# Kernel optimization log

Measured on AMD Instinct MI355X. Metric: run time of the kernel, lower is better.

The kernel has to match this reference:

```python
import jax, jax.numpy as jnp
import numpy as np

NB_ATOMS = 1024
NB_CHANNELS = 3
ATOM_SIZE = 16
NONDIFF_STEPS = 30
DIFF_STEPS = 10
TEMP = 100.0
EPS = 1e-8
BATCH = 16384


def setup_inputs() -> dict:
    key = jax.random.key(0)
    k1, k2 = jax.random.split(key)
    y = jax.random.normal(k1, (BATCH, NB_CHANNELS, ATOM_SIZE, ATOM_SIZE), dtype=jnp.float32)
    # init='random': randn / (atom_size * sqrt(nb_channels))
    atoms = jax.random.normal(k2, (NB_ATOMS, NB_CHANNELS, ATOM_SIZE, ATOM_SIZE), dtype=jnp.float32)
    atoms = atoms / (ATOM_SIZE * np.sqrt(NB_CHANNELS).astype(np.float32))
    return {"y": y, "atoms": atoms}


def reference(y, atoms):
    B = y.shape[0]
    A = atoms.shape[0]
    # L1 norms per sample / per atom
    y_norms = jnp.sum(jnp.abs(y.reshape(B, -1)), axis=1).reshape(-1, 1, 1, 1)  # [B,1,1,1]
    a_flat = atoms.reshape(A, -1)
    a_flat = a_flat / jnp.sum(jnp.abs(a_flat), axis=1, keepdims=True)          # [A,D]

    X = a_flat @ a_flat.T                                   # [A,A] gram matrix
    q = a_flat @ (y / y_norms).reshape(B, -1).T             # [A,B]
    coeffs = jnp.full((A, B), 1.0 / A, dtype=y.dtype)

    Xs = jax.lax.stop_gradient(X)
    qs = jax.lax.stop_gradient(q)

    def nondiff_step(i, c):
        grad = Xs @ c - qs                                  # [A,B]
        # faithful to torch: argmin over the BATCH dim, scatter one 1 per atom row
        am = jnp.zeros_like(c).at[jnp.arange(A), jnp.argmin(grad, axis=1)].set(1.0)
        d = am - c
        denom = jnp.sum(d * (Xs @ d)) + EPS                 # scalar (as in torch)
        lam = jnp.clip(-jnp.sum(d * grad, axis=0)[None, :] / denom, 0.0, 1.0)
        return c + d * lam

    coeffs = jax.lax.fori_loop(0, NONDIFF_STEPS, nondiff_step, coeffs)
    coeffs = jax.lax.stop_gradient(coeffs)

    def diff_step(c, _):
        grad = X @ c - q
        sm = jax.nn.softmax(-TEMP * grad, axis=0)           # softmax over atoms
        d = sm - c
        denom = jnp.sum(d * (X @ d)) + EPS
        lam = jnp.clip(-jnp.sum(d * grad, axis=0)[None, :] / denom, 0.0, 1.0)
        return c + d * lam, None

    coeffs, _ = jax.lax.scan(diff_step, coeffs, None, length=DIFF_STEPS)

    # einsum 'ij,ilmn->jlmn' with normalized atoms, rescale by y L1 norms
    recon = (coeffs.T @ a_flat).reshape(B, NB_CHANNELS, ATOM_SIZE, ATOM_SIZE) * y_norms
    return recon
```

## Files before the change

kernel.cpp:

```cpp
#include <hip/hip_runtime.h>
#include <hip/hip_bf16.h>
#include <math.h>

#define A_DIM 1024
#define D_DIM 768
#define B_DIM 16384
#define TEMP_C 100.0f
#define EPS_C 1e-8f


typedef __attribute__((ext_vector_type(8))) short short8;
typedef __attribute__((ext_vector_type(4))) float f32x4;
#define MFMA16(a, b, c) __builtin_amdgcn_mfma_f32_16x16x32_bf16(a, b, c, 0, 0, 0)

typedef __attribute__((address_space(3))) unsigned char lds_byte;
typedef __attribute__((address_space(1))) const unsigned char g_byte;
__device__ __forceinline__ void async_copy16(const void* gptr, void* lptr) {
    __builtin_amdgcn_global_load_lds((g_byte*)gptr, (lds_byte*)lptr, 16, 0, 0);
}

#define SCHED0 __builtin_amdgcn_sched_barrier(0)
#define ASM_BAR asm volatile("s_barrier" ::: "memory")

__device__ __forceinline__ void swz(int i, int& m0, int& n0) {
    int xcd = i & 7, j = i >> 3;
    m0 = ((xcd << 4) + (j >> 3)) << 7;
    n0 = (j & 7) << 7;
}


__device__ __forceinline__ float wave_sum(float v) {
#pragma unroll
    for (int m = 1; m < 64; m <<= 1) v += __shfl_xor(v, m);
    return v;
}
__device__ __forceinline__ float wave_max(float v) {
#pragma unroll
    for (int m = 1; m < 64; m <<= 1) v = fmaxf(v, __shfl_xor(v, m));
    return v;
}

__device__ __forceinline__ float block_reduce_sum(float v, float* red) {
    int t = threadIdx.x;
    v = wave_sum(v);
    if ((t & 63) == 0) red[t >> 6] = v;
    __syncthreads();
    float r = red[0] + red[1] + red[2] + red[3];
    __syncthreads();
    return r;
}

__device__ __forceinline__ float block_reduce_max(float v, float* red) {
    int t = threadIdx.x;
    v = wave_max(v);
    if ((t & 63) == 0) red[t >> 6] = v;
    __syncthreads();
    float r = fmaxf(fmaxf(red[0], red[1]), fmaxf(red[2], red[3]));
    __syncthreads();
    return r;
}

__device__ __forceinline__ void block_reduce_sum3(float& a, float& b, float& c, float* red) {
    int t = threadIdx.x;
    a = wave_sum(a);
    b = wave_sum(b);
    c = wave_sum(c);
    if ((t & 63) == 0) {
        int w = t >> 6;
        red[w] = a; red[4 + w] = b; red[8 + w] = c;
    }
    __syncthreads();
    a = red[0] + red[1] + red[2] + red[3];
    b = red[4] + red[5] + red[6] + red[7];
    c = red[8] + red[9] + red[10] + red[11];
    __syncthreads();
}


__device__ __forceinline__ unsigned int fkey(float v) {
    unsigned int u = __float_as_uint(v);
    return u ^ ((u & 0x80000000u) ? 0xFFFFFFFFu : 0x80000000u);
}

__device__ __forceinline__ unsigned short f2bf(float x) {
    unsigned int u = __float_as_uint(x);
    return (unsigned short)((u + 0x7FFFu + ((u >> 16) & 1u)) >> 16);
}
__device__ __forceinline__ float bf2f(unsigned short h) {
    return __uint_as_float(((unsigned int)h) << 16);
}
__device__ __forceinline__ void split2(float x, unsigned short& hi, unsigned short& lo) {
    hi = f2bf(x);
    lo = f2bf(x - bf2f(hi));
}


__device__ __forceinline__ void stage_tile8(const unsigned short* gsrc, int stride, int k0,
                                            unsigned short* ltile, int lane) {
    int srow = lane >> 2;
    int scol = (lane & 3) * 8;
#pragma unroll
    for (int s = 0; s < 8; s++) {
        const unsigned short* src = gsrc + (size_t)(s * 16 + srow) * stride + k0 + scol;
        async_copy16(src, ltile + s * 512);
    }
}

__device__ __forceinline__ void mfma_k32(const unsigned short* lds, int wm, int wn, int lane,
                                         f32x4 acc[4][4]) {
    int frow = lane & 15, fk = (lane >> 4) * 8;
    short8 ah[4], al[4], bh[4], bl[4];
#pragma unroll
    for (int t = 0; t < 4; t++) {
        int ar = (wm * 64 + t * 16 + frow) * 32 + fk;
        ah[t] = *(const short8*)&lds[ar];
        al[t] = *(const short8*)&lds[4096 + ar];
        int br = (wn * 64 + t * 16 + frow) * 32 + fk;
        bh[t] = *(const short8*)&lds[8192 + br];
        bl[t] = *(const short8*)&lds[12288 + br];
    }
#pragma unroll
    for (int i = 0; i < 4; i++)
#pragma unroll
        for (int j = 0; j < 4; j++) {
            acc[i][j] = MFMA16(ah[i], bh[j], acc[i][j]);
            acc[i][j] = MFMA16(ah[i], bl[j], acc[i][j]);
            acc[i][j] = MFMA16(al[i], bh[j], acc[i][j]);
        }
}


template <int PART>
__device__ __forceinline__ void stage_part(unsigned short* buf,
                                           const unsigned short* Ahi,
                                           const unsigned short* Alo,
                                           const unsigned short* Xhi,
                                           const unsigned short* Xlo,
                                           int m0, int n0, int k0, int t) {
    constexpr int AHI = 0;
    constexpr int ALO = 8192;
    constexpr int BHI = 16384;
    constexpr int BLO = 24576;
    int r = t >> 2;
    int cg = (t & 3) ^ ((t >> 3) & 3);
    size_t col = (size_t)k0 + cg * 8;
    if constexpr (PART == 0) {
        async_copy16(Ahi + (size_t)(m0 + r) * A_DIM + col,       buf + AHI + t * 8);
        async_copy16(Ahi + (size_t)(m0 + 128 + r) * A_DIM + col, buf + AHI + 4096 + t * 8);
    } else if constexpr (PART == 1) {
        async_copy16(Alo + (size_t)(m0 + r) * A_DIM + col,       buf + ALO + t * 8);
        async_copy16(Alo + (size_t)(m0 + 128 + r) * A_DIM + col, buf + ALO + 4096 + t * 8);
    } else if constexpr (PART == 2) {
        async_copy16(Xhi + (size_t)(n0 + r) * A_DIM + col,       buf + BHI + t * 8);
        async_copy16(Xhi + (size_t)(n0 + 128 + r) * A_DIM + col, buf + BHI + 4096 + t * 8);
    } else {
        async_copy16(Xlo + (size_t)(n0 + r) * A_DIM + col,       buf + BLO + t * 8);
        async_copy16(Xlo + (size_t)(n0 + 128 + r) * A_DIM + col, buf + BLO + 4096 + t * 8);
    }
}

__device__ __forceinline__ void mfma_mi3(short8 ah, short8 al,
                                         const short8 bh[4], const short8 bl[4],
                                         f32x4* accRow) {
#pragma unroll
    for (int j = 0; j < 4; j++) {
        accRow[j] = MFMA16(ah, bh[j], accRow[j]);
        accRow[j] = MFMA16(ah, bl[j], accRow[j]);
        accRow[j] = MFMA16(al, bh[j], accRow[j]);
    }
}

template <int MODE>
__global__ __launch_bounds__(512, 2) void gemm256(const unsigned short* __restrict__ Ahi,
                                                  const unsigned short* __restrict__ Alo,
                                                  const unsigned short* __restrict__ Xhi,
                                                  const unsigned short* __restrict__ Xlo,
                                                  const float* __restrict__ qt,
                                                  unsigned long long* __restrict__ keys,
                                                  float* __restrict__ cxc,
                                                  float* __restrict__ cq,
                                                  float* __restrict__ scal,
                                                  float* __restrict__ G,
                                                  float* __restrict__ scal3,
                                                  float* __restrict__ XC) {
    constexpr int BUFS = 32768;
    constexpr int AHI = 0;
    constexpr int ALO = 8192;
    constexpr int BHI = 16384;
    constexpr int BLO = 24576;
    __shared__ unsigned short lds[2 * BUFS];
    __shared__ float red[8];
    int tid = threadIdx.x;
    if (MODE == 0 && blockIdx.x == 0 && tid < 4) scal[tid] = 0.f;
    int w = tid >> 6, lane = tid & 63;
    int wm = w >> 2, wn = w & 3;
    int bi = blockIdx.x;
    int xcd = bi & 7, bj = bi >> 3;
    int m0 = ((xcd << 3) + (bj >> 2)) << 8;
    int n0 = (bj & 3) << 8;

    f32x4 acc[8][4];
#pragma unroll
    for (int i = 0; i < 8; i++)
#pragma unroll
        for (int j = 0; j < 4; j++) acc[i][j] = f32x4{0.f, 0.f, 0.f, 0.f};

    int frow = lane & 15;
    int sw = ((lane >> 4) ^ ((frow >> 1) & 3)) * 8;

    stage_part<0>(lds, Ahi, Alo, Xhi, Xlo, m0, n0, 0, tid);
    stage_part<1>(lds, Ahi, Alo, Xhi, Xlo, m0, n0, 0, tid);
    stage_part<2>(lds, Ahi, Alo, Xhi, Xlo, m0, n0, 0, tid);
    stage_part<3>(lds, Ahi, Alo, Xhi, Xlo, m0, n0, 0, tid);

    int cur = 0;
    for (int ks = 0; ks < 32; ++ks) {
        unsigned short* rb = lds + cur * BUFS;
        unsigned short* wb = lds + (cur ^ 1) * BUFS;
        const bool pf = (ks < 31);
        const int k1 = (ks + 1) * 32;

        if (pf) {
            stage_part<0>(wb, Ahi, Alo, Xhi, Xlo, m0, n0, k1, tid);
            SCHED0;
            asm volatile("s_waitcnt vmcnt(2)" ::: "memory");
        } else {
            asm volatile("s_waitcnt vmcnt(0)" ::: "memory");
        }
        SCHED0; ASM_BAR; SCHED0;

        short8 bh[4], bl[4];
#pragma unroll
        for (int j = 0; j < 4; j++) {
            int br = wn * 64 + j * 16 + frow;
            bh[j] = *(const short8*)&rb[BHI + br * 32 + sw];
            bl[j] = *(const short8*)&rb[BLO + br * 32 + sw];
        }
        {
            int ar0 = wm * 128 + 0 * 16 + frow, ar1 = wm * 128 + 1 * 16 + frow;
            short8 a0h = *(const short8*)&rb[AHI + ar0 * 32 + sw];
            short8 a1h = *(const short8*)&rb[AHI + ar1 * 32 + sw];
            short8 a0l = *(const short8*)&rb[ALO + ar0 * 32 + sw];
            short8 a1l = *(const short8*)&rb[ALO + ar1 * 32 + sw];
            if (pf) stage_part<1>(wb, Ahi, Alo, Xhi, Xlo, m0, n0, k1, tid);
            SCHED0; ASM_BAR; SCHED0;
            asm volatile("s_waitcnt lgkmcnt(0)" ::: "memory"); SCHED0;
            __builtin_amdgcn_s_setprio(1);
            mfma_mi3(a0h, a0l, bh, bl, acc[0]);
            mfma_mi3(a1h, a1l, bh, bl, acc[1]);
            __builtin_amdgcn_s_setprio(0);
            SCHED0; ASM_BAR; SCHED0;
        }
#pragma unroll
        for (int ph = 1; ph < 4; ph++) {
            int mia = 2 * ph, mib = 2 * ph + 1;
            int ara = wm * 128 + mia * 16 + frow, arb = wm * 128 + mib * 16 + frow;
            short8 aah = *(const short8*)&rb[AHI + ara * 32 + sw];
            short8 abh = *(const short8*)&rb[AHI + arb * 32 + sw];
            short8 aal = *(const short8*)&rb[ALO + ara * 32 + sw];
            short8 abl = *(const short8*)&rb[ALO + arb * 32 + sw];
            if (pf) {
                if (ph == 1) stage_part<2>(wb, Ahi, Alo, Xhi, Xlo, m0, n0, k1, tid);
                if (ph == 2) stage_part<3>(wb, Ahi, Alo, Xhi, Xlo, m0, n0, k1, tid);
            }
            SCHED0; ASM_BAR; SCHED0;
            asm volatile("s_waitcnt lgkmcnt(0)" ::: "memory"); SCHED0;
            __builtin_amdgcn_s_setprio(1);
            mfma_mi3(aah, aal, bh, bl, acc[mia]);
            mfma_mi3(abh, abl, bh, bl, acc[mib]);
            __builtin_amdgcn_s_setprio(0);
            SCHED0; ASM_BAR; SCHED0;
        }
        cur ^= 1;
    }

    int crow = (lane >> 4) * 4, ccol = lane & 15;
    if constexpr (MODE == 0) {
        unsigned long long best[4] = {~0ULL, ~0ULL, ~0ULL, ~0ULL};
#pragma unroll
        for (int mi = 0; mi < 8; mi++)
#pragma unroll
            for (int r = 0; r < 4; r++) {
                int gm = m0 + wm * 128 + mi * 16 + crow + r;
                float pcx = 0.f, pcq = 0.f;
#pragma unroll
                for (int jj = 0; jj < 4; jj++) {
                    int gn = n0 + wn * 64 + jj * 16 + ccol;
                    size_t idx = (size_t)gm * A_DIM + gn;
                    float c = bf2f(Ahi[idx]) + bf2f(Alo[idx]);
                    float q = qt[idx];
                    float xc = acc[mi][jj][r];
                    XC[idx] = xc;
                    pcx += c * xc;
                    pcq += c * q;
                    unsigned long long key =
                        ((unsigned long long)fkey(xc - q) << 32) | (unsigned int)gm;
                    if (key < best[jj]) best[jj] = key;
                }
                for (int mm = 1; mm < 16; mm <<= 1) {
                    pcx += __shfl_xor(pcx, mm, 16);
                    pcq += __shfl_xor(pcq, mm, 16);
                }
                if (ccol == 0) {
                    atomicAdd(&cxc[gm], pcx);
                    atomicAdd(&cq[gm], pcq);
                }
            }
#pragma unroll
        for (int jj = 0; jj < 4; jj++) {
            int gn = n0 + wn * 64 + jj * 16 + ccol;
            unsigned long long o = __shfl_xor(best[jj], 16);
            if (o < best[jj]) best[jj] = o;
            o = __shfl_xor(best[jj], 32);
            if (o < best[jj]) best[jj] = o;
            if ((lane >> 4) == 0) atomicMin(&keys[gn], best[jj]);
        }
    } else {
        float part = 0.f;
#pragma unroll
        for (int mi = 0; mi < 8; mi++)
#pragma unroll
            for (int r = 0; r < 4; r++) {
                int gm = m0 + wm * 128 + mi * 16 + crow + r;
#pragma unroll
                for (int jj = 0; jj < 4; jj++) {
                    int gn = n0 + wn * 64 + jj * 16 + ccol;
                    size_t idx = (size_t)gm * A_DIM + gn;
                    float d = bf2f(Ahi[idx]) + bf2f(Alo[idx]);
                    float xd = acc[mi][jj][r];
                    G[idx] = xd;
                    part += xd * d;
                }
            }
        part = wave_sum(part);
        if (lane == 0) red[w] = part;
        __syncthreads();
        if (tid == 0) {
            float tot = red[0] + red[1] + red[2] + red[3] +
                        red[4] + red[5] + red[6] + red[7];
            atomicAdd(scal3, tot);
        }
    }
}

__global__ __launch_bounds__(256) void grad_stream(const float* __restrict__ XC,
                                                   const float* __restrict__ qt,
                                                   const unsigned short* __restrict__ Chi,
                                                   const unsigned short* __restrict__ Clo,
                                                   unsigned long long* __restrict__ keys,
                                                   float* __restrict__ cxc,
                                                   float* __restrict__ cq,
                                                   float* __restrict__ scal) {
    __shared__ unsigned long long lkeys[4][1024];
    int tid = threadIdx.x;
    if (blockIdx.x == 0 && tid < 4) scal[tid] = 0.f;
    int w = tid >> 6, lane = tid & 63;
    int b0 = blockIdx.x * 64;

    unsigned long long best[16];
#pragma unroll
    for (int i = 0; i < 16; i++) best[i] = ~0ULL;

    for (int rr = 0; rr < 16; ++rr) {
        int b = b0 + w + rr * 4;
        const float* xcr = XC + (size_t)b * A_DIM;
        const float* qr  = qt + (size_t)b * A_DIM;
        const unsigned short* hr = Chi + (size_t)b * A_DIM;
        const unsigned short* lr = Clo + (size_t)b * A_DIM;
        float dx = 0.f, dq = 0.f;
#pragma unroll
        for (int ch = 0; ch < 4; ++ch) {
            int col = ch * 256 + lane * 4;
            float4 xv = *(const float4*)(xcr + col);
            float4 qv = *(const float4*)(qr + col);
            ushort4 hv = *(const ushort4*)(hr + col);
            ushort4 lv = *(const ushort4*)(lr + col);
            float c0 = bf2f(hv.x) + bf2f(lv.x);
            float c1 = bf2f(hv.y) + bf2f(lv.y);
            float c2 = bf2f(hv.z) + bf2f(lv.z);
            float c3 = bf2f(hv.w) + bf2f(lv.w);
            dx += c0 * xv.x + c1 * xv.y + c2 * xv.z + c3 * xv.w;
            dq += c0 * qv.x + c1 * qv.y + c2 * qv.z + c3 * qv.w;
            float g[4] = {xv.x - qv.x, xv.y - qv.y, xv.z - qv.z, xv.w - qv.w};
#pragma unroll
            for (int j = 0; j < 4; ++j) {
                unsigned long long key =
                    ((unsigned long long)fkey(g[j]) << 32) | (unsigned int)b;
                if (key < best[ch * 4 + j]) best[ch * 4 + j] = key;
            }
        }
        dx = wave_sum(dx);
        dq = wave_sum(dq);
        if (lane == 0) { cxc[b] = dx; cq[b] = dq; }
    }
#pragma unroll
    for (int ch = 0; ch < 4; ++ch)
#pragma unroll
        for (int j = 0; j < 4; ++j)
            lkeys[w][ch * 256 + lane * 4 + j] = best[ch * 4 + j];
    __syncthreads();
    for (int i = tid; i < 1024; i += 256) {
        unsigned long long v = lkeys[0][i];
        if (lkeys[1][i] < v) v = lkeys[1][i];
        if (lkeys[2][i] < v) v = lkeys[2][i];
        if (lkeys[3][i] < v) v = lkeys[3][i];
        atomicMin(&keys[i], v);
    }
}


__global__ __launch_bounds__(256) void ynorm_split_kernel(const float* __restrict__ y,
                                                          float* __restrict__ ynorm,
                                                          unsigned short* __restrict__ Ynh,
                                                          unsigned short* __restrict__ Ynl) {
    __shared__ float red[16];
    int b = blockIdx.x;
    const float* row = y + (size_t)b * D_DIM;
    float s = 0.f;
    for (int i = threadIdx.x; i < D_DIM; i += 256) s += fabsf(row[i]);
    float tot = block_reduce_sum(s, red);
    float inv = 1.f / tot;
    unsigned short* oh = Ynh + (size_t)b * D_DIM;
    unsigned short* ol = Ynl + (size_t)b * D_DIM;
    for (int i = threadIdx.x; i < D_DIM; i += 256) {
        unsigned short h, l;
        split2(row[i] * inv, h, l);
        oh[i] = h; ol[i] = l;
    }
    if (threadIdx.x == 0) ynorm[b] = tot;
}

__global__ __launch_bounds__(256) void anorm_kernel(const float* __restrict__ atoms,
                                                    float* __restrict__ an,
                                                    float* __restrict__ anrm,
                                                    unsigned short* __restrict__ Anh,
                                                    unsigned short* __restrict__ Anl) {
    __shared__ float red[16];
    int a = blockIdx.x;
    const float* row = atoms + (size_t)a * D_DIM;
    float s = 0.f;
    for (int i = threadIdx.x; i < D_DIM; i += 256) s += fabsf(row[i]);
    float tot = block_reduce_sum(s, red);
    float inv = 1.f / tot;
    for (int i = threadIdx.x; i < D_DIM; i += 256) {
        float v = row[i] * inv;
        an[(size_t)a * D_DIM + i] = v;
        unsigned short h, l;
        split2(v, h, l);
        Anh[(size_t)a * D_DIM + i] = h;
        Anl[(size_t)a * D_DIM + i] = l;
    }
    if (threadIdx.x == 0) anrm[a] = tot;
}

__global__ __launch_bounds__(256) void atrans_split_kernel(const float* __restrict__ atoms,
                                                           const float* __restrict__ anrm,
                                                           unsigned short* __restrict__ AnTh,
                                                           unsigned short* __restrict__ AnTl) {
    int n = blockIdx.x;
    for (int k = threadIdx.x; k < A_DIM; k += 256) {
        float v = atoms[(size_t)k * D_DIM + n] / anrm[k];
        unsigned short h, l;
        split2(v, h, l);
        AnTh[(size_t)n * A_DIM + k] = h;
        AnTl[(size_t)n * A_DIM + k] = l;
    }
}

__global__ __launch_bounds__(256) void split_kernel(const float* __restrict__ src,
                                                    unsigned short* __restrict__ hi,
                                                    unsigned short* __restrict__ lo,
                                                    int n4) {
    int i = blockIdx.x * 256 + threadIdx.x;
    if (i < n4) {
        float4 v = ((const float4*)src)[i];
        ushort4 h, l;
        split2(v.x, h.x, l.x);
        split2(v.y, h.y, l.y);
        split2(v.z, h.z, l.z);
        split2(v.w, h.w, l.w);
        ((ushort4*)hi)[i] = h;
        ((ushort4*)lo)[i] = l;
    }
}

__global__ __launch_bounds__(256) void fill_pair_kernel(unsigned short* __restrict__ Chi,
                                                        unsigned short* __restrict__ Clo,
                                                        size_t n4) {
    size_t i = (size_t)blockIdx.x * 256 + threadIdx.x;
    if (i < n4) {
        unsigned short h, l;
        split2(1.f / A_DIM, h, l);
        ((ushort4*)Chi)[i] = make_ushort4(h, h, h, h);
        ((ushort4*)Clo)[i] = make_ushort4(l, l, l, l);
    }
}

__global__ __launch_bounds__(256) void gemm_xt(const float* __restrict__ Aop,
                                               float* __restrict__ Cout) {
    const int LDT = 132;
    const int N = A_DIM, K = D_DIM;
    __shared__ float As[16 * LDT];
    __shared__ float Bs[16 * LDT];
    int m0 = blockIdx.y * 128, n0 = blockIdx.x * 128;
    int tid = threadIdx.x;
    int tx = tid & 15, ty = tid >> 4;
    float acc[8][8];
#pragma unroll
    for (int i = 0; i < 8; i++)
#pragma unroll
        for (int j = 0; j < 8; j++) acc[i][j] = 0.f;
    for (int k0 = 0; k0 < K; k0 += 16) {
#pragma unroll
        for (int s = 0; s < 2; s++) {
            int idx = tid + s * 256;
            int row = idx >> 2, kq = (idx & 3) * 4;
            float4 v = *(const float4*)(Aop + (size_t)(m0 + row) * K + k0 + kq);
            As[(kq + 0) * LDT + row] = v.x;
            As[(kq + 1) * LDT + row] = v.y;
            As[(kq + 2) * LDT + row] = v.z;
            As[(kq + 3) * LDT + row] = v.w;
        }
#pragma unroll
        for (int s = 0; s < 2; s++) {
            int idx = tid + s * 256;
            int row = idx >> 2, kq = (idx & 3) * 4;
            float4 v = *(const float4*)(Aop + (size_t)(n0 + row) * K + k0 + kq);
            Bs[(kq + 0) * LDT + row] = v.x;
            Bs[(kq + 1) * LDT + row] = v.y;
            Bs[(kq + 2) * LDT + row] = v.z;
            Bs[(kq + 3) * LDT + row] = v.w;
        }
        __syncthreads();
#pragma unroll
        for (int kk = 0; kk < 16; kk++) {
            float a[8], b[8];
            *(float4*)(a)     = *(const float4*)(As + kk * LDT + ty * 8);
            *(float4*)(a + 4) = *(const float4*)(As + kk * LDT + ty * 8 + 4);
            *(float4*)(b)     = *(const float4*)(Bs + kk * LDT + tx * 8);
            *(float4*)(b + 4) = *(const float4*)(Bs + kk * LDT + tx * 8 + 4);
#pragma unroll
            for (int i = 0; i < 8; i++)
#pragma unroll
                for (int j = 0; j < 8; j++) acc[i][j] = fmaf(a[i], b[j], acc[i][j]);
        }
        __syncthreads();
    }
#pragma unroll
    for (int i = 0; i < 8; i++) {
        int row = m0 + ty * 8 + i;
#pragma unroll
        for (int j = 0; j < 8; j += 4) {
            int col = n0 + tx * 8 + j;
            float4 v = make_float4(acc[i][j], acc[i][j + 1], acc[i][j + 2], acc[i][j + 3]);
            *(float4*)(Cout + (size_t)row * N + col) = v;
        }
    }
}

__global__ __launch_bounds__(256) void qt_mfma(const unsigned short* __restrict__ Ynh,
                                               const unsigned short* __restrict__ Ynl,
                                               const unsigned short* __restrict__ Anh,
                                               const unsigned short* __restrict__ Anl,
                                               float* __restrict__ qt) {
    __shared__ unsigned short lds[16384];
    int tid = threadIdx.x;
    int w = tid >> 6, lane = tid & 63;
    int wm = w >> 1, wn = w & 1;
    int m0, n0;
    swz(blockIdx.x, m0, n0);

    f32x4 acc[4][4];
#pragma unroll
    for (int i = 0; i < 4; i++)
#pragma unroll
        for (int j = 0; j < 4; j++) acc[i][j] = f32x4{0.f, 0.f, 0.f, 0.f};

    const unsigned short* gsrc;
    if (w == 0) gsrc = Ynh + (size_t)m0 * D_DIM;
    else if (w == 1) gsrc = Ynl + (size_t)m0 * D_DIM;
    else if (w == 2) gsrc = Anh + (size_t)n0 * D_DIM;
    else gsrc = Anl + (size_t)n0 * D_DIM;
    unsigned short* ltile = lds + w * 4096;
    for (int k0 = 0; k0 < D_DIM; k0 += 32) {
        stage_tile8(gsrc, D_DIM, k0, ltile, lane);
        __syncthreads();
        mfma_k32(lds, wm, wn, lane, acc);
        __syncthreads();
    }

    int crow = (lane >> 4) * 4, ccol = lane & 15;
#pragma unroll
    for (int i = 0; i < 4; i++) {
        int gm = m0 + wm * 64 + i * 16 + crow;
#pragma unroll
        for (int j = 0; j < 4; j++) {
            int gn = n0 + wn * 64 + j * 16 + ccol;
#pragma unroll
            for (int r = 0; r < 4; r++)
                qt[(size_t)(gm + r) * A_DIM + gn] = acc[i][j][r];
        }
    }
}


__global__ __launch_bounds__(256) void init_kernel(unsigned long long* __restrict__ keys,
                                                   float* __restrict__ num_amg,
                                                   float* __restrict__ cxc,
                                                   float* __restrict__ cq,
                                                   float* __restrict__ scal) {
    int i = blockIdx.x * 256 + threadIdx.x;
    num_amg[i] = 0.f;
    cxc[i] = 0.f;
    cq[i] = 0.f;
    if (i < A_DIM) keys[i] = ~0ULL;
    if (i < 4) scal[i] = 0.f;
}

__global__ __launch_bounds__(256) void stats_kernel(const float* __restrict__ Xf,
                                                    const unsigned long long* __restrict__ keys,
                                                    const unsigned short* __restrict__ Chi,
                                                    const unsigned short* __restrict__ Clo,
                                                    const float* __restrict__ qt,
                                                    const float* __restrict__ cxc,
                                                    int* __restrict__ bstar,
                                                    float* __restrict__ num_amg,
                                                    float* __restrict__ scal) {
    __shared__ float red[16];
    int a = blockIdx.x;
    int ba = (int)(unsigned int)(keys[a] & 0xFFFFFFFFULL);
    const float* xr = Xf + (size_t)a * A_DIM;
    const unsigned short* ch = Chi + (size_t)ba * A_DIM;
    const unsigned short* cl = Clo + (size_t)ba * A_DIM;
    float ps = 0.f, xs = 0.f;
    for (int i = threadIdx.x; i < A_DIM; i += 256) {
        float xv = xr[i];
        if ((int)(unsigned int)(keys[i] & 0xFFFFFFFFULL) == ba) ps += xv;
        xs += xv * (bf2f(ch[i]) + bf2f(cl[i]));
    }
    float s1p = (threadIdx.x < 16) ? cxc[(a << 4) + threadIdx.x] : 0.f;
    block_reduce_sum3(ps, xs, s1p, red);
    if (threadIdx.x == 0) {
        bstar[a] = ba;
        atomicAdd(&scal[0], ps);
        atomicAdd(&scal[2], xs);
        atomicAdd(&scal[1], s1p);
        atomicAdd(&num_amg[ba], xs - qt[(size_t)ba * A_DIM + a]);
    }
}

__global__ __launch_bounds__(256) void ndupdate_kernel(unsigned short* __restrict__ Chi,
                                                       unsigned short* __restrict__ Clo,
                                                       const int* __restrict__ bstar,
                                                       float* __restrict__ cxc,
                                                       float* __restrict__ cq,
                                                       float* __restrict__ num_amg,
                                                       const float* __restrict__ scal,
                                                       unsigned long long* __restrict__ keys,
                                                       float* __restrict__ XC,
                                                       const float* __restrict__ Xf) {
    __shared__ int mlist[1024];
    __shared__ int mcount;
    int b = blockIdx.x;
    int i = threadIdx.x;
    if (i == 0) mcount = 0;
    float den = scal[0] + scal[1] - 2.f * scal[2] + EPS_C;
    float lam = fminf(fmaxf((cxc[b] - cq[b] - num_amg[b]) / den, 0.f), 1.f);
    float om = 1.f - lam;
    ushort4* h4 = (ushort4*)(Chi + (size_t)b * A_DIM);
    ushort4* l4 = (ushort4*)(Clo + (size_t)b * A_DIM);
    ushort4 h = h4[i], l = l4[i];
    int4 bs = ((const int4*)bstar)[i];
    float c0 = om * (bf2f(h.x) + bf2f(l.x)) + ((bs.x == b) ? lam : 0.f);
    float c1 = om * (bf2f(h.y) + bf2f(l.y)) + ((bs.y == b) ? lam : 0.f);
    float c2 = om * (bf2f(h.z) + bf2f(l.z)) + ((bs.z == b) ? lam : 0.f);
    float c3 = om * (bf2f(h.w) + bf2f(l.w)) + ((bs.w == b) ? lam : 0.f);
    split2(c0, h.x, l.x);
    split2(c1, h.y, l.y);
    split2(c2, h.z, l.z);
    split2(c3, h.w, l.w);
    h4[i] = h; l4[i] = l;
    __syncthreads();
    for (int a = i; a < A_DIM; a += 256)
        if (bstar[a] == b) { int p = atomicAdd(&mcount, 1); mlist[p] = a; }
    __syncthreads();
    float4 xv = *(float4*)(XC + (size_t)b * A_DIM + i * 4);
    xv.x *= om; xv.y *= om; xv.z *= om; xv.w *= om;
    int mc = mcount;
    for (int m = 0; m < mc; m++) {
        float4 av = *(const float4*)(Xf + (size_t)mlist[m] * A_DIM + i * 4);
        xv.x += lam * av.x; xv.y += lam * av.y;
        xv.z += lam * av.z; xv.w += lam * av.w;
    }
    *(float4*)(XC + (size_t)b * A_DIM + i * 4) = xv;
    __syncthreads();
    if (i == 0) {
        cxc[b] = 0.f;
        cq[b] = 0.f;
        num_amg[b] = 0.f;
        if (b < A_DIM) keys[b] = ~0ULL;
    }
}


__global__ __launch_bounds__(256) void rinit_kernel(float* __restrict__ XC,
                                                    const float* __restrict__ qt) {
    size_t i = (size_t)blockIdx.x * 256 + threadIdx.x;
    float4 x = ((const float4*)XC)[i];
    float4 q = ((const float4*)qt)[i];
    x.x -= q.x; x.y -= q.y; x.z -= q.z; x.w -= q.w;
    ((float4*)XC)[i] = x;
}

__global__ __launch_bounds__(256) void softmax_kernel(const float* __restrict__ R,
                                                      unsigned short* __restrict__ Chi,
                                                      unsigned short* __restrict__ Clo,
                                                      float* __restrict__ num_cg,
                                                      float* __restrict__ scal3) {
    __shared__ float red[16];
    int b = blockIdx.x;
    int i = threadIdx.x;
    if (b == 0 && i == 0) *scal3 = 0.f;
    const float4* g4 = (const float4*)(R + (size_t)b * A_DIM);
    ushort4* h4 = (ushort4*)(Chi + (size_t)b * A_DIM);
    ushort4* l4 = (ushort4*)(Clo + (size_t)b * A_DIM);
    float4 g = g4[i];
    ushort4 h = h4[i], l = l4[i];
    float c0 = bf2f(h.x) + bf2f(l.x);
    float c1 = bf2f(h.y) + bf2f(l.y);
    float c2 = bf2f(h.z) + bf2f(l.z);
    float c3 = bf2f(h.w) + bf2f(l.w);
    float4 t = make_float4(-TEMP_C * g.x, -TEMP_C * g.y, -TEMP_C * g.z, -TEMP_C * g.w);
    float m = fmaxf(fmaxf(t.x, t.y), fmaxf(t.z, t.w));
    float M = block_reduce_max(m, red);
    float4 e = make_float4(expf(t.x - M), expf(t.y - M), expf(t.z - M), expf(t.w - M));
    float S = block_reduce_sum(e.x + e.y + e.z + e.w, red);
    float inv = 1.f / S;
    float4 sm = make_float4(e.x * inv, e.y * inv, e.z * inv, e.w * inv);
    float np = (c0 - sm.x) * g.x + (c1 - sm.y) * g.y + (c2 - sm.z) * g.z + (c3 - sm.w) * g.w;
    split2(sm.x - c0, h.x, l.x);
    split2(sm.y - c1, h.y, l.y);
    split2(sm.z - c2, h.z, l.z);
    split2(sm.w - c3, h.w, l.w);
    h4[i] = h; l4[i] = l;
    float nt = block_reduce_sum(np, red);
    if (i == 0) num_cg[b] = nt;
}

__global__ __launch_bounds__(256) void dupdate_kernel(float* __restrict__ R,
                                                      const float* __restrict__ Xd,
                                                      unsigned short* __restrict__ Chi,
                                                      unsigned short* __restrict__ Clo,
                                                      const float* __restrict__ num_cg,
                                                      const float* __restrict__ scal3) {
    __shared__ float red[16];
    int b = blockIdx.x;
    int i = threadIdx.x;
    float4* r4 = (float4*)(R + (size_t)b * A_DIM);
    float4 g = r4[i];
    float4 t = make_float4(-TEMP_C * g.x, -TEMP_C * g.y, -TEMP_C * g.z, -TEMP_C * g.w);
    float m = fmaxf(fmaxf(t.x, t.y), fmaxf(t.z, t.w));
    float M = block_reduce_max(m, red);
    float4 e = make_float4(expf(t.x - M), expf(t.y - M), expf(t.z - M), expf(t.w - M));
    float S = block_reduce_sum(e.x + e.y + e.z + e.w, red);
    float inv = 1.f / S;
    float4 sm = make_float4(e.x * inv, e.y * inv, e.z * inv, e.w * inv);
    float den = *scal3 + EPS_C;
    float lam = fminf(fmaxf(num_cg[b] / den, 0.f), 1.f);
    float om = 1.f - lam;
    ushort4* h4 = (ushort4*)(Chi + (size_t)b * A_DIM);
    ushort4* l4 = (ushort4*)(Clo + (size_t)b * A_DIM);
    ushort4 h = h4[i], l = l4[i];
    float c0 = sm.x - om * (bf2f(h.x) + bf2f(l.x));
    float c1 = sm.y - om * (bf2f(h.y) + bf2f(l.y));
    float c2 = sm.z - om * (bf2f(h.z) + bf2f(l.z));
    float c3 = sm.w - om * (bf2f(h.w) + bf2f(l.w));
    split2(c0, h.x, l.x);
    split2(c1, h.y, l.y);
    split2(c2, h.z, l.z);
    split2(c3, h.w, l.w);
    h4[i] = h; l4[i] = l;
    float4 xd = ((const float4*)(Xd + (size_t)b * A_DIM))[i];
    g.x += lam * xd.x; g.y += lam * xd.y;
    g.z += lam * xd.z; g.w += lam * xd.w;
    r4[i] = g;
}

__global__ __launch_bounds__(256) void mfma_recon(const unsigned short* __restrict__ Chi,
                                                  const unsigned short* __restrict__ Clo,
                                                  const unsigned short* __restrict__ AnTh,
                                                  const unsigned short* __restrict__ AnTl,
                                                  const float* __restrict__ ynorm,
                                                  float* __restrict__ out) {
    __shared__ unsigned short lds[16384];
    int tid = threadIdx.x;
    int w = tid >> 6, lane = tid & 63;
    int wm = w >> 1, wn = w & 1;
    int m0 = blockIdx.y * 128, n0 = blockIdx.x * 128;

    f32x4 acc[4][4];
#pragma unroll
    for (int i = 0; i < 4; i++)
#pragma unroll
        for (int j = 0; j < 4; j++) acc[i][j] = f32x4{0.f, 0.f, 0.f, 0.f};

    const unsigned short* gsrc;
    if (w == 0) gsrc = Chi + (size_t)m0 * A_DIM;
    else if (w == 1) gsrc = Clo + (size_t)m0 * A_DIM;
    else if (w == 2) gsrc = AnTh + (size_t)n0 * A_DIM;
    else gsrc = AnTl + (size_t)n0 * A_DIM;
    unsigned short* ltile = lds + w * 4096;
    for (int k0 = 0; k0 < A_DIM; k0 += 32) {
        stage_tile8(gsrc, A_DIM, k0, ltile, lane);
        __syncthreads();
        mfma_k32(lds, wm, wn, lane, acc);
        __syncthreads();
    }

    int crow = (lane >> 4) * 4, ccol = lane & 15;
#pragma unroll
    for (int i = 0; i < 4; i++) {
        int gm = m0 + wm * 64 + i * 16 + crow;
#pragma unroll
        for (int j = 0; j < 4; j++) {
            int gn = n0 + wn * 64 + j * 16 + ccol;
#pragma unroll
            for (int r = 0; r < 4; r++)
                out[(size_t)(gm + r) * D_DIM + gn] = acc[i][j][r] * ynorm[gm + r];
        }
    }
}


extern "C" void kernel_launch(void* const* d_in, const int* in_sizes, int n_in,
                              void* d_out, int out_size, void* d_ws, size_t ws_size,
                              hipStream_t stream) {
    const float* y = (const float*)d_in[0];
    const float* atoms = (const float*)d_in[1];
    float* out = (float*)d_out;

    char* ws = (char*)d_ws;
    size_t off = 0;
    auto alloc = [&](size_t bytes) -> void* {
        void* p = ws + off;
        off += (bytes + 255) & ~(size_t)255;
        return p;
    };
    const size_t BA = (size_t)B_DIM * A_DIM;
    unsigned short* Chi = (unsigned short*)alloc(BA * 2);
    unsigned short* Clo = (unsigned short*)alloc(BA * 2);
    float* Greg = (float*)alloc(BA * 4);
    float* qt = (float*)alloc(BA * 4);
    unsigned short* Xhi = (unsigned short*)alloc((size_t)A_DIM * A_DIM * 2);
    unsigned short* Xlo = (unsigned short*)alloc((size_t)A_DIM * A_DIM * 2);
    float* Xf = (float*)alloc((size_t)A_DIM * A_DIM * 4);
    float* ynorm = (float*)alloc(B_DIM * 4);
    float* anrm  = (float*)alloc(A_DIM * 4);
    float* cxc   = (float*)alloc(B_DIM * 4);
    float* cq    = (float*)alloc(B_DIM * 4);
    float* num_amg = (float*)alloc(B_DIM * 4);
    float* num_cg  = (float*)alloc(B_DIM * 4);
    unsigned long long* keys = (unsigned long long*)alloc(A_DIM * 8);
    int* bstar = (int*)alloc(A_DIM * 4);
    float* scal = (float*)alloc(256);
    (void)ws_size; (void)in_sizes; (void)n_in; (void)out_size;

    float* an = Greg;
    unsigned short* Anh = (unsigned short*)(an + (size_t)A_DIM * D_DIM);
    unsigned short* Anl = Anh + (size_t)A_DIM * D_DIM;
    unsigned short* Ynh = Anl + (size_t)A_DIM * D_DIM;
    unsigned short* Ynl = Ynh + (size_t)B_DIM * D_DIM;
    float* XC = Greg;
    float* R  = Greg;
    float* Xd = qt;
    unsigned short* AnTh = (unsigned short*)Greg;
    unsigned short* AnTl = (unsigned short*)Greg + (size_t)D_DIM * A_DIM;

    ynorm_split_kernel<<<B_DIM, 256, 0, stream>>>(y, ynorm, Ynh, Ynl);
    anorm_kernel<<<A_DIM, 256, 0, stream>>>(atoms, an, anrm, Anh, Anl);
    gemm_xt<<<dim3(A_DIM / 128, A_DIM / 128), 256, 0, stream>>>(an, Xf);
    split_kernel<<<A_DIM * A_DIM / 4 / 256, 256, 0, stream>>>(Xf, Xhi, Xlo, A_DIM * A_DIM / 4);
    qt_mfma<<<1024, 256, 0, stream>>>(Ynh, Ynl, Anh, Anl, qt);
    fill_pair_kernel<<<(int)(BA / 4 / 256), 256, 0, stream>>>(Chi, Clo, BA / 4);
    init_kernel<<<B_DIM / 256, 256, 0, stream>>>(keys, num_amg, cxc, cq, scal);

    for (int it = 0; it < 30; it++) {
        if ((it & 7) == 0)
            gemm256<0><<<256, 512, 0, stream>>>(Chi, Clo, Xhi, Xlo, qt,
                                                keys, cxc, cq, scal, nullptr, nullptr, XC);
        else
            grad_stream<<<256, 256, 0, stream>>>(XC, qt, Chi, Clo, keys, cxc, cq, scal);
        stats_kernel<<<A_DIM, 256, 0, stream>>>(Xf, keys, Chi, Clo, qt, cxc,
                                                bstar, num_amg, scal);
        ndupdate_kernel<<<B_DIM, 256, 0, stream>>>(Chi, Clo, bstar, cxc, cq,
                                                   num_amg, scal, keys, XC, Xf);
    }

    rinit_kernel<<<(int)(BA / 4 / 256), 256, 0, stream>>>(XC, qt);
    for (int it = 0; it < 10; it++) {
        softmax_kernel<<<B_DIM, 256, 0, stream>>>(R, Chi, Clo, num_cg, &scal[3]);
        gemm256<3><<<256, 512, 0, stream>>>(Chi, Clo, Xhi, Xlo, nullptr,
                                            nullptr, nullptr, nullptr, nullptr,
                                            Xd, &scal[3], nullptr);
        dupdate_kernel<<<B_DIM, 256, 0, stream>>>(R, Xd, Chi, Clo, num_cg, &scal[3]);
    }

    atrans_split_kernel<<<D_DIM, 256, 0, stream>>>(atoms, anrm, AnTh, AnTl);
    mfma_recon<<<dim3(D_DIM / 128, B_DIM / 128), 256, 0, stream>>>(Chi, Clo, AnTh, AnTl,
                                                                   ynorm, out);
}
```

Measured before the change: 6.145 ms.

## Fuse Frank-Wolfe coefficient update into next gradient pass, fuse softmax into diff update

The non-differentiable loop now applies the previous step's coefficient and XC update inside the streaming gradient kernel (fgrad), using double-buffered argmin keys and scalar accumulators. The standalone ndupdate pass runs only before each full GEMM refresh and at the end. The diff loop fuses the next iteration's softmax and numerator computation into dupdate, removing one full-batch kernel per step. The aim is to cut repeated reads and writes of the B×A coefficient and gradient arrays and reduce launches. The cost is more complex buffer-parity bookkeeping and per-row ballot and mask work in fgrad.

```diff
diff --git a/kernel.cpp b/kernel.cpp
--- a/kernel.cpp
+++ b/kernel.cpp
@@ -92,6 +92,9 @@
 __device__ __forceinline__ void split2(float x, unsigned short& hi, unsigned short& lo) {
     hi = f2bf(x);
     lo = f2bf(x - bf2f(hi));
+}
+__device__ __forceinline__ float clamp01(float x) {
+    return fminf(fmaxf(x, 0.f), 1.f);
 }
 
 
@@ -343,19 +346,28 @@
     }
 }
 
-__global__ __launch_bounds__(256) void grad_stream(const float* __restrict__ XC,
-                                                   const float* __restrict__ qt,
-                                                   const unsigned short* __restrict__ Chi,
-                                                   const unsigned short* __restrict__ Clo,
-                                                   unsigned long long* __restrict__ keys,
-                                                   float* __restrict__ cxc,
-                                                   float* __restrict__ cq,
-                                                   float* __restrict__ scal) {
+__global__ __launch_bounds__(256) void fgrad(const float* __restrict__ qt,
+                                             unsigned short* __restrict__ Chi,
+                                             unsigned short* __restrict__ Clo,
+                                             float* __restrict__ XC,
+                                             const float* __restrict__ Xf,
+                                             const unsigned long long* __restrict__ Kprev,
+                                             unsigned long long* __restrict__ Kcur,
+                                             float* __restrict__ cxc,
+                                             float* __restrict__ cq,
+                                             float* __restrict__ num_amg,
+                                             const float* __restrict__ scalPrev,
+                                             float* __restrict__ scalCur) {
     __shared__ unsigned long long lkeys[4][1024];
     int tid = threadIdx.x;
-    if (blockIdx.x == 0 && tid < 4) scal[tid] = 0.f;
+    if (blockIdx.x == 0 && tid < 4) scalCur[tid] = 0.f;
     int w = tid >> 6, lane = tid & 63;
     int b0 = blockIdx.x * 64;
+    float den = scalPrev[0] + scalPrev[1] - 2.f * scalPrev[2] + EPS_C;
+
+    unsigned int klow[16];
+#pragma unroll
+    for (int s = 0; s < 16; s++) klow[s] = (unsigned int)Kprev[lane + s * 64];
 
     unsigned long long best[16];
 #pragma unroll
@@ -363,35 +375,72 @@
 
     for (int rr = 0; rr < 16; ++rr) {
         int b = b0 + w + rr * 4;
-        const float* xcr = XC + (size_t)b * A_DIM;
-        const float* qr  = qt + (size_t)b * A_DIM;
-        const unsigned short* hr = Chi + (size_t)b * A_DIM;
-        const unsigned short* lr = Clo + (size_t)b * A_DIM;
+        float lam = clamp01((cxc[b] - cq[b] - num_amg[b]) / den);
+        float om = 1.f - lam;
+        unsigned long long mask[16];
+#pragma unroll
+        for (int s = 0; s < 16; s++) mask[s] = __ballot(klow[s] == (unsigned int)b);
+
+        unsigned short* hr = Chi + (size_t)b * A_DIM;
+        unsigned short* lr = Clo + (size_t)b * A_DIM;
+        float* xcr = XC + (size_t)b * A_DIM;
+        const float* qr = qt + (size_t)b * A_DIM;
         float dx = 0.f, dq = 0.f;
 #pragma unroll
         for (int ch = 0; ch < 4; ++ch) {
             int col = ch * 256 + lane * 4;
+            ushort4 hv = *(const ushort4*)(hr + col);
+            ushort4 lv = *(const ushort4*)(lr + col);
             float4 xv = *(const float4*)(xcr + col);
             float4 qv = *(const float4*)(qr + col);
-            ushort4 hv = *(const ushort4*)(hr + col);
-            ushort4 lv = *(const ushort4*)(lr + col);
-            float c0 = bf2f(hv.x) + bf2f(lv.x);
-            float c1 = bf2f(hv.y) + bf2f(lv.y);
-            float c2 = bf2f(hv.z) + bf2f(lv.z);
-            float c3 = bf2f(hv.w) + bf2f(lv.w);
+            int sel = lane >> 4;
+            unsigned long long mw =
+                (sel == 0) ? mask[ch * 4 + 0] :
+                (sel == 1) ? mask[ch * 4 + 1] :
+                (sel == 2) ? mask[ch * 4 + 2] : mask[ch * 4 + 3];
+            unsigned int ind4 = (unsigned int)((mw >> ((lane & 15) * 4)) & 0xFULL);
+            float c0 = om * (bf2f(hv.x) + bf2f(lv.x)) + ((ind4 & 1u) ? lam : 0.f);
+            float c1 = om * (bf2f(hv.y) + bf2f(lv.y)) + ((ind4 & 2u) ? lam : 0.f);
+            float c2 = om * (bf2f(hv.z) + bf2f(lv.z)) + ((ind4 & 4u) ? lam : 0.f);
+            float c3 = om * (bf2f(hv.w) + bf2f(lv.w)) + ((ind4 & 8u) ? lam : 0.f);
+            xv.x *= om; xv.y *= om; xv.z *= om; xv.w *= om;
+#pragma unroll
+            for (int s = 0; s < 16; s++) {
+                unsigned long long m = mask[s];
+                while (m) {
+                    int a = __ffsll(m) - 1 + s * 64;
+                    m &= m - 1;
+                    float4 av = *(const float4*)(Xf + (size_t)a * A_DIM + col);
+                    xv.x += lam * av.x; xv.y += lam * av.y;
+                    xv.z += lam * av.z; xv.w += lam * av.w;
+                }
+            }
+            split2(c0, hv.x, lv.x);
+            split2(c1, hv.y, lv.y);
+            split2(c2, hv.z, lv.z);
+            split2(c3, hv.w, lv.w);
+            *(ushort4*)(hr + col) = hv;
+            *(ushort4*)(lr + col) = lv;
+            *(float4*)(xcr + col) = xv;
+            float g0 = xv.x - qv.x, g1 = xv.y - qv.y, g2 = xv.z - qv.z, g3 = xv.w - qv.w;
             dx += c0 * xv.x + c1 * xv.y + c2 * xv.z + c3 * xv.w;
             dq += c0 * qv.x + c1 * qv.y + c2 * qv.z + c3 * qv.w;
-            float g[4] = {xv.x - qv.x, xv.y - qv.y, xv.z - qv.z, xv.w - qv.w};
-#pragma unroll
-            for (int j = 0; j < 4; ++j) {
-                unsigned long long key =
-                    ((unsigned long long)fkey(g[j]) << 32) | (unsigned int)b;
-                if (key < best[ch * 4 + j]) best[ch * 4 + j] = key;
-            }
+            unsigned long long k0 = ((unsigned long long)fkey(g0) << 32) | (unsigned int)b;
+            unsigned long long k1 = ((unsigned long long)fkey(g1) << 32) | (unsigned int)b;
+            unsigned long long k2 = ((unsigned long long)fkey(g2) << 32) | (unsigned int)b;
+            unsigned long long k3 = ((unsigned long long)fkey(g3) << 32) | (unsigned int)b;
+            if (k0 < best[ch * 4 + 0]) best[ch * 4 + 0] = k0;
+            if (k1 < best[ch * 4 + 1]) best[ch * 4 + 1] = k1;
+            if (k2 < best[ch * 4 + 2]) best[ch * 4 + 2] = k2;
+            if (k3 < best[ch * 4 + 3]) best[ch * 4 + 3] = k3;
         }
         dx = wave_sum(dx);
         dq = wave_sum(dq);
-        if (lane == 0) { cxc[b] = dx; cq[b] = dq; }
+        if (lane == 0) {
+            cxc[b] = dx;
+            cq[b] = dq;
+            num_amg[b] = 0.f;
+        }
     }
 #pragma unroll
     for (int ch = 0; ch < 4; ++ch)
@@ -404,7 +453,7 @@
         if (lkeys[1][i] < v) v = lkeys[1][i];
         if (lkeys[2][i] < v) v = lkeys[2][i];
         if (lkeys[3][i] < v) v = lkeys[3][i];
-        atomicMin(&keys[i], v);
+        atomicMin(&Kcur[i], v);
     }
 }
 
@@ -613,68 +662,106 @@
     num_amg[i] = 0.f;
     cxc[i] = 0.f;
     cq[i] = 0.f;
-    if (i < A_DIM) keys[i] = ~0ULL;
-    if (i < 4) scal[i] = 0.f;
+    if (i < 2 * A_DIM) keys[i] = ~0ULL;
+    if (i < 8) scal[i] = 0.f;
 }
 
 __global__ __launch_bounds__(256) void stats_kernel(const float* __restrict__ Xf,
-                                                    const unsigned long long* __restrict__ keys,
+                                                    const unsigned long long* __restrict__ Kcur,
                                                     const unsigned short* __restrict__ Chi,
                                                     const unsigned short* __restrict__ Clo,
                                                     const float* __restrict__ qt,
                                                     const float* __restrict__ cxc,
-                                                    int* __restrict__ bstar,
                                                     float* __restrict__ num_amg,
-                                                    float* __restrict__ scal) {
+                                                    float* __restrict__ scalCur,
+                                                    unsigned long long* __restrict__ Knext) {
     __shared__ float red[16];
     int a = blockIdx.x;
-    int ba = (int)(unsigned int)(keys[a] & 0xFFFFFFFFULL);
+    int ba = (int)(unsigned int)(Kcur[a] & 0xFFFFFFFFULL);
     const float* xr = Xf + (size_t)a * A_DIM;
     const unsigned short* ch = Chi + (size_t)ba * A_DIM;
     const unsigned short* cl = Clo + (size_t)ba * A_DIM;
     float ps = 0.f, xs = 0.f;
     for (int i = threadIdx.x; i < A_DIM; i += 256) {
         float xv = xr[i];
-        if ((int)(unsigned int)(keys[i] & 0xFFFFFFFFULL) == ba) ps += xv;
+        if ((int)(unsigned int)(Kcur[i] & 0xFFFFFFFFULL) == ba) ps += xv;
         xs += xv * (bf2f(ch[i]) + bf2f(cl[i]));
     }
     float s1p = (threadIdx.x < 16) ? cxc[(a << 4) + threadIdx.x] : 0.f;
     block_reduce_sum3(ps, xs, s1p, red);
     if (threadIdx.x == 0) {
-        bstar[a] = ba;
-        atomicAdd(&scal[0], ps);
-        atomicAdd(&scal[2], xs);
-        atomicAdd(&scal[1], s1p);
+        atomicAdd(&scalCur[0], ps);
+        atomicAdd(&scalCur[2], xs);
+        atomicAdd(&scalCur[1], s1p);
         atomicAdd(&num_amg[ba], xs - qt[(size_t)ba * A_DIM + a]);
-    }
-}
-
-__global__ __launch_bounds__(256) void ndupdate_kernel(unsigned short* __restrict__ Chi,
-                                                       unsigned short* __restrict__ Clo,
-                                                       const int* __restrict__ bstar,
-                                                       float* __restrict__ cxc,
-                                                       float* __restrict__ cq,
-                                                       float* __restrict__ num_amg,
-                                                       const float* __restrict__ scal,
-                                                       unsigned long long* __restrict__ keys,
-                                                       float* __restrict__ XC,
-                                                       const float* __restrict__ Xf) {
+        Knext[a] = ~0ULL;
+    }
+}
+
+__global__ __launch_bounds__(256) void ndupdate_c(unsigned short* __restrict__ Chi,
+                                                  unsigned short* __restrict__ Clo,
+                                                  const unsigned long long* __restrict__ Kprev,
+                                                  float* __restrict__ cxc,
+                                                  float* __restrict__ cq,
+                                                  float* __restrict__ num_amg,
+                                                  const float* __restrict__ scalPrev) {
+    int b = blockIdx.x;
+    float den = scalPrev[0] + scalPrev[1] - 2.f * scalPrev[2] + EPS_C;
+    float lam = clamp01((cxc[b] - cq[b] - num_amg[b]) / den);
+    float om = 1.f - lam;
+    int i = threadIdx.x;
+    ushort4* h4 = (ushort4*)(Chi + (size_t)b * A_DIM);
+    ushort4* l4 = (ushort4*)(Clo + (size_t)b * A_DIM);
+    ushort4 h = h4[i], l = l4[i];
+    int b0 = (int)(unsigned int)Kprev[i * 4 + 0];
+    int b1 = (int)(unsigned int)Kprev[i * 4 + 1];
+    int b2 = (int)(unsigned int)Kprev[i * 4 + 2];
+    int b3 = (int)(unsigned int)Kprev[i * 4 + 3];
+    float c0 = om * (bf2f(h.x) + bf2f(l.x)) + ((b0 == b) ? lam : 0.f);
+    float c1 = om * (bf2f(h.y) + bf2f(l.y)) + ((b1 == b) ? lam : 0.f);
+    float c2 = om * (bf2f(h.z) + bf2f(l.z)) + ((b2 == b) ? lam : 0.f);
+    float c3 = om * (bf2f(h.w) + bf2f(l.w)) + ((b3 == b) ? lam : 0.f);
+    split2(c0, h.x, l.x);
+    split2(c1, h.y, l.y);
+    split2(c2, h.z, l.z);
+    split2(c3, h.w, l.w);
+    h4[i] = h; l4[i] = l;
+    __syncthreads();
+    if (i == 0) {
+        cxc[b] = 0.f;
+        cq[b] = 0.f;
+        num_amg[b] = 0.f;
+    }
+}
+
+__global__ __launch_bounds__(256) void ndupdate_full(unsigned short* __restrict__ Chi,
+                                                     unsigned short* __restrict__ Clo,
+                                                     const unsigned long long* __restrict__ Kprev,
+                                                     const float* __restrict__ cxc,
+                                                     const float* __restrict__ cq,
+                                                     const float* __restrict__ num_amg,
+                                                     const float* __restrict__ scalPrev,
+                                                     float* __restrict__ XC,
+                                                     const float* __restrict__ Xf) {
     __shared__ int mlist[1024];
     __shared__ int mcount;
     int b = blockIdx.x;
     int i = threadIdx.x;
     if (i == 0) mcount = 0;
-    float den = scal[0] + scal[1] - 2.f * scal[2] + EPS_C;
-    float lam = fminf(fmaxf((cxc[b] - cq[b] - num_amg[b]) / den, 0.f), 1.f);
+    float den = scalPrev[0] + scalPrev[1] - 2.f * scalPrev[2] + EPS_C;
+    float lam = clamp01((cxc[b] - cq[b] - num_amg[b]) / den);
     float om = 1.f - lam;
     ushort4* h4 = (ushort4*)(Chi + (size_t)b * A_DIM);
     ushort4* l4 = (ushort4*)(Clo + (size_t)b * A_DIM);
     ushort4 h = h4[i], l = l4[i];
-    int4 bs = ((const int4*)bstar)[i];
-    float c0 = om * (bf2f(h.x) + bf2f(l.x)) + ((bs.x == b) ? lam : 0.f);
-    float c1 = om * (bf2f(h.y) + bf2f(l.y)) + ((bs.y == b) ? lam : 0.f);
-    float c2 = om * (bf2f(h.z) + bf2f(l.z)) + ((bs.z == b) ? lam : 0.f);
-    float c3 = om * (bf2f(h.w) + bf2f(l.w)) + ((bs.w == b) ? lam : 0.f);
+    int b0 = (int)(unsigned int)Kprev[i * 4 + 0];
+    int b1 = (int)(unsigned int)Kprev[i * 4 + 1];
+    int b2 = (int)(unsigned int)Kprev[i * 4 + 2];
+    int b3 = (int)(unsigned int)Kprev[i * 4 + 3];
+    float c0 = om * (bf2f(h.x) + bf2f(l.x)) + ((b0 == b) ? lam : 0.f);
+    float c1 = om * (bf2f(h.y) + bf2f(l.y)) + ((b1 == b) ? lam : 0.f);
+    float c2 = om * (bf2f(h.z) + bf2f(l.z)) + ((b2 == b) ? lam : 0.f);
+    float c3 = om * (bf2f(h.w) + bf2f(l.w)) + ((b3 == b) ? lam : 0.f);
     split2(c0, h.x, l.x);
     split2(c1, h.y, l.y);
     split2(c2, h.z, l.z);
@@ -682,7 +769,7 @@
     h4[i] = h; l4[i] = l;
     __syncthreads();
     for (int a = i; a < A_DIM; a += 256)
-        if (bstar[a] == b) { int p = atomicAdd(&mcount, 1); mlist[p] = a; }
+        if ((int)(unsigned int)Kprev[a] == b) { int p = atomicAdd(&mcount, 1); mlist[p] = a; }
     __syncthreads();
     float4 xv = *(float4*)(XC + (size_t)b * A_DIM + i * 4);
     xv.x *= om; xv.y *= om; xv.z *= om; xv.w *= om;
@@ -693,13 +780,6 @@
         xv.z += lam * av.z; xv.w += lam * av.w;
     }
     *(float4*)(XC + (size_t)b * A_DIM + i * 4) = xv;
-    __syncthreads();
-    if (i == 0) {
-        cxc[b] = 0.f;
-        cq[b] = 0.f;
-        num_amg[b] = 0.f;
-        if (b < A_DIM) keys[b] = ~0ULL;
-    }
 }
 
 
@@ -747,15 +827,18 @@
     if (i == 0) num_cg[b] = nt;
 }
 
-__global__ __launch_bounds__(256) void dupdate_kernel(float* __restrict__ R,
-                                                      const float* __restrict__ Xd,
-                                                      unsigned short* __restrict__ Chi,
-                                                      unsigned short* __restrict__ Clo,
-                                                      const float* __restrict__ num_cg,
-                                                      const float* __restrict__ scal3) {
+template <int LAST>
+__global__ __launch_bounds__(256) void dupdate_fused(float* __restrict__ R,
+                                                     const float* __restrict__ Xd,
+                                                     unsigned short* __restrict__ Chi,
+                                                     unsigned short* __restrict__ Clo,
+                                                     float* __restrict__ num_cg,
+                                                     const float* __restrict__ s3cur,
+                                                     float* __restrict__ s3next) {
     __shared__ float red[16];
     int b = blockIdx.x;
     int i = threadIdx.x;
+    if (!LAST && b == 0 && i == 0) *s3next = 0.f;
     float4* r4 = (float4*)(R + (size_t)b * A_DIM);
     float4 g = r4[i];
     float4 t = make_float4(-TEMP_C * g.x, -TEMP_C * g.y, -TEMP_C * g.z, -TEMP_C * g.w);
@@ -765,8 +848,8 @@
     float S = block_reduce_sum(e.x + e.y + e.z + e.w, red);
     float inv = 1.f / S;
     float4 sm = make_float4(e.x * inv, e.y * inv, e.z * inv, e.w * inv);
-    float den = *scal3 + EPS_C;
-    float lam = fminf(fmaxf(num_cg[b] / den, 0.f), 1.f);
+    float den = *s3cur + EPS_C;
+    float lam = clamp01(num_cg[b] / den);
     float om = 1.f - lam;
     ushort4* h4 = (ushort4*)(Chi + (size_t)b * A_DIM);
     ushort4* l4 = (ushort4*)(Clo + (size_t)b * A_DIM);
@@ -775,15 +858,35 @@
     float c1 = sm.y - om * (bf2f(h.y) + bf2f(l.y));
     float c2 = sm.z - om * (bf2f(h.z) + bf2f(l.z));
     float c3 = sm.w - om * (bf2f(h.w) + bf2f(l.w));
-    split2(c0, h.x, l.x);
-    split2(c1, h.y, l.y);
-    split2(c2, h.z, l.z);
-    split2(c3, h.w, l.w);
-    h4[i] = h; l4[i] = l;
     float4 xd = ((const float4*)(Xd + (size_t)b * A_DIM))[i];
     g.x += lam * xd.x; g.y += lam * xd.y;
     g.z += lam * xd.z; g.w += lam * xd.w;
     r4[i] = g;
+    if (LAST) {
+        split2(c0, h.x, l.x);
+        split2(c1, h.y, l.y);
+        split2(c2, h.z, l.z);
+        split2(c3, h.w, l.w);
+        h4[i] = h; l4[i] = l;
+    } else {
+        float4 t2 = make_float4(-TEMP_C * g.x, -TEMP_C * g.y, -TEMP_C * g.z, -TEMP_C * g.w);
+        float m2 = fmaxf(fmaxf(t2.x, t2.y), fmaxf(t2.z, t2.w));
+        float M2 = block_reduce_max(m2, red);
+        float4 e2 = make_float4(expf(t2.x - M2), expf(t2.y - M2),
+                                expf(t2.z - M2), expf(t2.w - M2));
+        float S2 = block_reduce_sum(e2.x + e2.y + e2.z + e2.w, red);
+        float inv2 = 1.f / S2;
+        float4 sm2 = make_float4(e2.x * inv2, e2.y * inv2, e2.z * inv2, e2.w * inv2);
+        float np = (c0 - sm2.x) * g.x + (c1 - sm2.y) * g.y +
+                   (c2 - sm2.z) * g.z + (c3 - sm2.w) * g.w;
+        split2(sm2.x - c0, h.x, l.x);
+        split2(sm2.y - c1, h.y, l.y);
+        split2(sm2.z - c2, h.z, l.z);
+        split2(sm2.w - c3, h.w, l.w);
+        h4[i] = h; l4[i] = l;
+        float nt = block_reduce_sum(np, red);
+        if (i == 0) num_cg[b] = nt;
+    }
 }
 
 __global__ __launch_bounds__(256) void mfma_recon(const unsigned short* __restrict__ Chi,
@@ -860,8 +963,7 @@
     float* cq    = (float*)alloc(B_DIM * 4);
     float* num_amg = (float*)alloc(B_DIM * 4);
     float* num_cg  = (float*)alloc(B_DIM * 4);
-    unsigned long long* keys = (unsigned long long*)alloc(A_DIM * 8);
-    int* bstar = (int*)alloc(A_DIM * 4);
+    unsigned long long* keys = (unsigned long long*)alloc(2 * A_DIM * 8);
     float* scal = (float*)alloc(256);
     (void)ws_size; (void)in_sizes; (void)n_in; (void)out_size;
 
@@ -884,25 +986,44 @@
     fill_pair_kernel<<<(int)(BA / 4 / 256), 256, 0, stream>>>(Chi, Clo, BA / 4);
     init_kernel<<<B_DIM / 256, 256, 0, stream>>>(keys, num_amg, cxc, cq, scal);
 
-    for (int it = 0; it < 30; it++) {
-        if ((it & 7) == 0)
+    for (int t = 0; t < 30; t++) {
+        int cur = t & 1, prev = 1 - cur;
+        unsigned long long* Kcur = keys + cur * A_DIM;
+        unsigned long long* Kprev = keys + prev * A_DIM;
+        unsigned long long* Knext = keys + ((t + 1) & 1) * A_DIM;
+        float* sCur = scal + cur * 4;
+        float* sPrev = scal + prev * 4;
+        if ((t & 7) == 0) {
             gemm256<0><<<256, 512, 0, stream>>>(Chi, Clo, Xhi, Xlo, qt,
-                                                keys, cxc, cq, scal, nullptr, nullptr, XC);
-        else
-            grad_stream<<<256, 256, 0, stream>>>(XC, qt, Chi, Clo, keys, cxc, cq, scal);
-        stats_kernel<<<A_DIM, 256, 0, stream>>>(Xf, keys, Chi, Clo, qt, cxc,
-                                                bstar, num_amg, scal);
-        ndupdate_kernel<<<B_DIM, 256, 0, stream>>>(Chi, Clo, bstar, cxc, cq,
-                                                   num_amg, scal, keys, XC, Xf);
+                                                Kcur, cxc, cq, scal, nullptr, nullptr, XC);
+        } else {
+            fgrad<<<256, 256, 0, stream>>>(qt, Chi, Clo, XC, Xf, Kprev, Kcur,
+                                           cxc, cq, num_amg, sPrev, sCur);
+        }
+        stats_kernel<<<A_DIM, 256, 0, stream>>>(Xf, Kcur, Chi, Clo, qt, cxc,
+                                                num_amg, sCur, Knext);
+        if (t == 7 || t == 15 || t == 23)
+            ndupdate_c<<<B_DIM, 256, 0, stream>>>(Chi, Clo, Kcur, cxc, cq,
+                                                  num_amg, sCur);
+        if (t == 29)
+            ndupdate_full<<<B_DIM, 256, 0, stream>>>(Chi, Clo, Kcur, cxc, cq,
+                                                     num_amg, sCur, XC, Xf);
     }
 
     rinit_kernel<<<(int)(BA / 4 / 256), 256, 0, stream>>>(XC, qt);
-    for (int it = 0; it < 10; it++) {
-        softmax_kernel<<<B_DIM, 256, 0, stream>>>(R, Chi, Clo, num_cg, &scal[3]);
+    softmax_kernel<<<B_DIM, 256, 0, stream>>>(R, Chi, Clo, num_cg, &scal[3]);
+    for (int t = 0; t < 10; t++) {
+        float* s3cur = &scal[3 + (t & 1) * 4];
+        float* s3next = &scal[3 + ((t + 1) & 1) * 4];
         gemm256<3><<<256, 512, 0, stream>>>(Chi, Clo, Xhi, Xlo, nullptr,
                                             nullptr, nullptr, nullptr, nullptr,
-                                            Xd, &scal[3], nullptr);
-        dupdate_kernel<<<B_DIM, 256, 0, stream>>>(R, Xd, Chi, Clo, num_cg, &scal[3]);
+                                            Xd, s3cur, nullptr);
+        if (t < 9)
+            dupdate_fused<0><<<B_DIM, 256, 0, stream>>>(R, Xd, Chi, Clo, num_cg,
+                                                        s3cur, s3next);
+        else
+            dupdate_fused<1><<<B_DIM, 256, 0, stream>>>(R, Xd, Chi, Clo, num_cg,
+                                                        s3cur, nullptr);
     }
 
     atrans_split_kernel<<<D_DIM, 256, 0, stream>>>(atoms, anrm, AnTh, AnTl);
```

New measurement: 5.600 ms. 1.1x faster.
